# Kernel optimization log

Measured on AMD Instinct MI355X. Metric: run time of the kernel, lower is better.

Reference implementation:

```python
import jax, jax.numpy as jnp
import numpy as np


def setup_inputs() -> dict:
    key = jax.random.key(0)
    k1, k2 = jax.random.split(key)
    B, S, D, E = 4, 4096, 2048, 64
    x = jax.random.normal(k1, (B, S, D), dtype=jnp.float32)
    # nn.Linear default init ~ U(-1/sqrt(D), 1/sqrt(D)); scale down for stability
    w_gate = jax.random.normal(k2, (E, D), dtype=jnp.float32) * (1.0 / np.sqrt(D))
    expert_bias = jnp.zeros((E,), dtype=jnp.float32)
    return {"x": x, "w_gate": w_gate, "expert_bias": expert_bias}


def reference(x, w_gate, expert_bias):
    # gate_logits: [B, S, E]
    gate_logits = jnp.einsum('bsd,ed->bse', x, w_gate)
    gate_weights = jax.nn.sigmoid(gate_logits)
    biased_logits = gate_logits + expert_bias
    k = 8  # num_experts_per_tok
    _, topk_indices = jax.lax.top_k(biased_logits, k)  # [B, S, k]
    topk_weights = jnp.take_along_axis(gate_weights, topk_indices, axis=-1)
    topk_weights = topk_weights / jnp.sum(topk_weights, axis=-1, keepdims=True)
    return topk_weights, topk_indices
```

## Files before the change

kernel.cpp:

```cpp
#include <hip/hip_runtime.h>
#include <math.h>

#define DDIM 2048
#define NE 64
#define TOPK 8
#define RB 32
#define KSEG 512
#define NKT (KSEG / 32)

typedef float f32x4 __attribute__((ext_vector_type(4)));
typedef short short8 __attribute__((ext_vector_type(8)));
typedef __bf16 bf16x8 __attribute__((ext_vector_type(8)));
typedef unsigned int uint;

__device__ __forceinline__ void split3(float f, short& h, short& m, short& l) {
    uint u = __builtin_bit_cast(uint, f);
    h = (short)(u >> 16);
    float r = f - __builtin_bit_cast(float, u & 0xffff0000u);
    uint ur = __builtin_bit_cast(uint, r);
    m = (short)(ur >> 16);
    float r2 = r - __builtin_bit_cast(float, ur & 0xffff0000u);
    l = (short)(__builtin_bit_cast(uint, r2) >> 16);
}

__global__ void wsplit_kernel(const float* __restrict__ w, short* __restrict__ wh,
                              short* __restrict__ wm, short* __restrict__ wl) {
    int tid = blockIdx.x * 256 + threadIdx.x;
    size_t base = (size_t)tid * 8;
    short8 hs, ms, ls;
#pragma unroll
    for (int j = 0; j < 8; ++j) {
        short h, m, l;
        split3(w[base + j], h, m, l);
        hs[j] = h; ms[j] = m; ls[j] = l;
    }
    *(short8*)&wh[base] = hs;
    *(short8*)&wm[base] = ms;
    *(short8*)&wl[base] = ls;
}

__global__ __launch_bounds__(256, 2) void gate_kernel(
    const float* __restrict__ x,
    const float* __restrict__ bias,
    const short* __restrict__ wh,
    const short* __restrict__ wm,
    const short* __restrict__ wl,
    float* __restrict__ out_w,
    float* __restrict__ out_i)
{
    __shared__ float slab[4][RB][NE];
    __shared__ float logits[RB][NE + 1];

    const int t    = threadIdx.x;
    const int lane = t & 63;
    const int wv   = t >> 6;
    const int rl   = lane & 15;
    const int kg   = lane >> 4;
    const int row0 = blockIdx.x * RB;
    const int kbase = wv * KSEG;

    f32x4 acc[2][4];
#pragma unroll
    for (int rt = 0; rt < 2; ++rt)
#pragma unroll
        for (int et = 0; et < 4; ++et) acc[rt][et] = (f32x4){0.f, 0.f, 0.f, 0.f};

    const float* xb = x + (size_t)(row0 + rl) * DDIM + kbase + kg * 8;
    const int    wo = rl * DDIM + kbase + kg * 8;

    for (int kt = 0; kt < NKT; ++kt) {
        const int ko = kt * 32;

        bf16x8 ah[2], am[2], al[2];
#pragma unroll
        for (int rt = 0; rt < 2; ++rt) {
            const float* xp = xb + (size_t)(rt * 16) * DDIM + ko;
            f32x4 a0 = *(const f32x4*)xp;
            f32x4 a1 = *(const f32x4*)(xp + 4);
            short8 hs, ms, ls;
#pragma unroll
            for (int j = 0; j < 4; ++j) {
                short h, m, l;
                split3(a0[j], h, m, l);
                hs[j] = h; ms[j] = m; ls[j] = l;
                split3(a1[j], h, m, l);
                hs[j + 4] = h; ms[j + 4] = m; ls[j + 4] = l;
            }
            ah[rt] = __builtin_bit_cast(bf16x8, hs);
            am[rt] = __builtin_bit_cast(bf16x8, ms);
            al[rt] = __builtin_bit_cast(bf16x8, ls);
        }

#pragma unroll
        for (int et = 0; et < 4; ++et) {
            const int bofs = et * 16 * DDIM + wo + ko;
            bf16x8 bh = __builtin_bit_cast(bf16x8, *(const short8*)&wh[bofs]);
            bf16x8 bm = __builtin_bit_cast(bf16x8, *(const short8*)&wm[bofs]);
            bf16x8 bl = __builtin_bit_cast(bf16x8, *(const short8*)&wl[bofs]);
#pragma unroll
            for (int rt = 0; rt < 2; ++rt) {
                acc[rt][et] = __builtin_amdgcn_mfma_f32_16x16x32_bf16(ah[rt], bh, acc[rt][et], 0, 0, 0);
                acc[rt][et] = __builtin_amdgcn_mfma_f32_16x16x32_bf16(ah[rt], bm, acc[rt][et], 0, 0, 0);
                acc[rt][et] = __builtin_amdgcn_mfma_f32_16x16x32_bf16(am[rt], bh, acc[rt][et], 0, 0, 0);
                acc[rt][et] = __builtin_amdgcn_mfma_f32_16x16x32_bf16(am[rt], bm, acc[rt][et], 0, 0, 0);
                acc[rt][et] = __builtin_amdgcn_mfma_f32_16x16x32_bf16(ah[rt], bl, acc[rt][et], 0, 0, 0);
                acc[rt][et] = __builtin_amdgcn_mfma_f32_16x16x32_bf16(al[rt], bh, acc[rt][et], 0, 0, 0);
            }
        }
    }

#pragma unroll
    for (int rt = 0; rt < 2; ++rt)
#pragma unroll
        for (int et = 0; et < 4; ++et)
#pragma unroll
            for (int r = 0; r < 4; ++r)
                slab[wv][rt * 16 + kg * 4 + r][et * 16 + rl] = acc[rt][et][r];
    __syncthreads();

#pragma unroll
    for (int i = 0; i < 8; ++i) {
        int idx = t * 8 + i;
        int r = idx >> 6, cc = idx & 63;
        logits[r][cc] = slab[0][r][cc] + slab[1][r][cc] + slab[2][r][cc] + slab[3][r][cc];
    }
    __syncthreads();

    const float bias_l = bias[lane];
    for (int r8 = 0; r8 < 8; ++r8) {
        const int r  = wv * 8 + r8;
        const int gr = row0 + r;
        float raw = logits[r][lane];
        float sig = 1.f / (1.f + expf(-raw));
        float vv  = raw + bias_l;

        float wsum = 0.f, myw = 0.f;
        int   myidx = 0;
#pragma unroll
        for (int k = 0; k < TOPK; ++k) {
            float m = vv;
#pragma unroll
            for (int off = 32; off; off >>= 1)
                m = fmaxf(m, __shfl_xor(m, off));
            unsigned long long b = __ballot(vv == m);
            int idx = (int)__builtin_ctzll(b);
            float wk = __shfl(sig, idx);
            wsum += wk;
            if (lane == k)  { myw = wk; myidx = idx; }
            if (lane == idx) vv = -INFINITY;
        }
        if (lane < TOPK) {
            out_w[(size_t)gr * TOPK + lane] = myw / wsum;
            out_i[(size_t)gr * TOPK + lane] = (float)myidx;
        }
    }
}

extern "C" void kernel_launch(void* const* d_in, const int* in_sizes, int n_in,
                              void* d_out, int out_size, void* d_ws, size_t ws_size,
                              hipStream_t stream) {
    const float* x    = (const float*)d_in[0];
    const float* w    = (const float*)d_in[1];
    const float* bias = (const float*)d_in[2];
    const int NR = in_sizes[0] / DDIM;
    float* out   = (float*)d_out;
    float* out_w = out;
    float* out_i = out + (size_t)NR * TOPK;

    short* wh = (short*)d_ws;
    short* wm = wh + (size_t)NE * DDIM;
    short* wl = wm + (size_t)NE * DDIM;

    hipLaunchKernelGGL(wsplit_kernel, dim3(NE * DDIM / (256 * 8)), dim3(256), 0, stream,
                       w, wh, wm, wl);
    hipLaunchKernelGGL(gate_kernel, dim3(NR / RB), dim3(256), 0, stream,
                       x, bias, wh, wm, wl, out_w, out_i);
}
```

Measured before the change: 83.50 us.

## Halve row block, double-buffer loads, pad slab, interleave top-k rows

Shrinks the per-block row tile from 32 to 16, which doubles the grid so more waves are resident, and halves accumulator registers. The K loop now uses explicit double buffering: the x and split weight loads for the next step are issued before the current step's MFMAs. The slab is padded to avoid LDS bank conflicts. The top-k selection processes four rows at once so their shuffle reductions can overlap. In exchange, each weight fragment is reused across fewer rows, which doubles total weight traffic from L2, and the prefetch buffers add register pressure.

```diff
diff --git a/kernel.cpp b/kernel.cpp
--- a/kernel.cpp
+++ b/kernel.cpp
@@ -4,7 +4,7 @@
 #define DDIM 2048
 #define NE 64
 #define TOPK 8
-#define RB 32
+#define RB 16
 #define KSEG 512
 #define NKT (KSEG / 32)
 
@@ -48,7 +48,7 @@
     float* __restrict__ out_w,
     float* __restrict__ out_i)
 {
-    __shared__ float slab[4][RB][NE];
+    __shared__ float slab[4][RB][NE + 2];
     __shared__ float logits[RB][NE + 1];
 
     const int t    = threadIdx.x;
@@ -59,99 +59,115 @@
     const int row0 = blockIdx.x * RB;
     const int kbase = wv * KSEG;
 
-    f32x4 acc[2][4];
+    f32x4 acc[4];
 #pragma unroll
-    for (int rt = 0; rt < 2; ++rt)
-#pragma unroll
-        for (int et = 0; et < 4; ++et) acc[rt][et] = (f32x4){0.f, 0.f, 0.f, 0.f};
+    for (int et = 0; et < 4; ++et) acc[et] = (f32x4){0.f, 0.f, 0.f, 0.f};
 
-    const float* xb = x + (size_t)(row0 + rl) * DDIM + kbase + kg * 8;
-    const int    wo = rl * DDIM + kbase + kg * 8;
+    const float* xb  = x  + (size_t)(row0 + rl) * DDIM + kbase + kg * 8;
+    const short* whb = wh + (size_t)rl * DDIM + kbase + kg * 8;
+    const short* wmb = wm + (size_t)rl * DDIM + kbase + kg * 8;
+    const short* wlb = wl + (size_t)rl * DDIM + kbase + kg * 8;
 
-    for (int kt = 0; kt < NKT; ++kt) {
-        const int ko = kt * 32;
+    f32x4 Aa0, Aa1, Ba0, Ba1;
+    short8 Abh[4], Abm[4], Abl[4], Bbh[4], Bbm[4], Bbl[4];
 
-        bf16x8 ah[2], am[2], al[2];
-#pragma unroll
-        for (int rt = 0; rt < 2; ++rt) {
-            const float* xp = xb + (size_t)(rt * 16) * DDIM + ko;
-            f32x4 a0 = *(const f32x4*)xp;
-            f32x4 a1 = *(const f32x4*)(xp + 4);
-            short8 hs, ms, ls;
-#pragma unroll
-            for (int j = 0; j < 4; ++j) {
-                short h, m, l;
-                split3(a0[j], h, m, l);
-                hs[j] = h; ms[j] = m; ls[j] = l;
-                split3(a1[j], h, m, l);
-                hs[j + 4] = h; ms[j + 4] = m; ls[j + 4] = l;
-            }
-            ah[rt] = __builtin_bit_cast(bf16x8, hs);
-            am[rt] = __builtin_bit_cast(bf16x8, ms);
-            al[rt] = __builtin_bit_cast(bf16x8, ls);
-        }
+#define LOADT(P, ko_)                                                          \
+    {                                                                          \
+        P##a0 = *(const f32x4*)(xb + (ko_));                                   \
+        P##a1 = *(const f32x4*)(xb + (ko_) + 4);                               \
+        _Pragma("unroll")                                                      \
+        for (int et = 0; et < 4; ++et) {                                       \
+            P##bh[et] = *(const short8*)&whb[et * 16 * DDIM + (ko_)];          \
+            P##bm[et] = *(const short8*)&wmb[et * 16 * DDIM + (ko_)];          \
+            P##bl[et] = *(const short8*)&wlb[et * 16 * DDIM + (ko_)];          \
+        }                                                                      \
+    }
 
-#pragma unroll
-        for (int et = 0; et < 4; ++et) {
-            const int bofs = et * 16 * DDIM + wo + ko;
-            bf16x8 bh = __builtin_bit_cast(bf16x8, *(const short8*)&wh[bofs]);
-            bf16x8 bm = __builtin_bit_cast(bf16x8, *(const short8*)&wm[bofs]);
-            bf16x8 bl = __builtin_bit_cast(bf16x8, *(const short8*)&wl[bofs]);
-#pragma unroll
-            for (int rt = 0; rt < 2; ++rt) {
-                acc[rt][et] = __builtin_amdgcn_mfma_f32_16x16x32_bf16(ah[rt], bh, acc[rt][et], 0, 0, 0);
-                acc[rt][et] = __builtin_amdgcn_mfma_f32_16x16x32_bf16(ah[rt], bm, acc[rt][et], 0, 0, 0);
-                acc[rt][et] = __builtin_amdgcn_mfma_f32_16x16x32_bf16(am[rt], bh, acc[rt][et], 0, 0, 0);
-                acc[rt][et] = __builtin_amdgcn_mfma_f32_16x16x32_bf16(am[rt], bm, acc[rt][et], 0, 0, 0);
-                acc[rt][et] = __builtin_amdgcn_mfma_f32_16x16x32_bf16(ah[rt], bl, acc[rt][et], 0, 0, 0);
-                acc[rt][et] = __builtin_amdgcn_mfma_f32_16x16x32_bf16(al[rt], bh, acc[rt][et], 0, 0, 0);
-            }
-        }
+#define COMPUTE(P)                                                             \
+    {                                                                          \
+        short8 hs, ms, ls;                                                     \
+        _Pragma("unroll")                                                      \
+        for (int j = 0; j < 4; ++j) {                                          \
+            short h_, m_, l_;                                                  \
+            split3(P##a0[j], h_, m_, l_); hs[j] = h_; ms[j] = m_; ls[j] = l_;  \
+            split3(P##a1[j], h_, m_, l_); hs[j+4] = h_; ms[j+4] = m_; ls[j+4] = l_; \
+        }                                                                      \
+        bf16x8 ah = __builtin_bit_cast(bf16x8, hs);                            \
+        bf16x8 am = __builtin_bit_cast(bf16x8, ms);                            \
+        bf16x8 al = __builtin_bit_cast(bf16x8, ls);                            \
+        _Pragma("unroll")                                                      \
+        for (int et = 0; et < 4; ++et) {                                       \
+            bf16x8 bh = __builtin_bit_cast(bf16x8, P##bh[et]);                 \
+            bf16x8 bm = __builtin_bit_cast(bf16x8, P##bm[et]);                 \
+            bf16x8 bl = __builtin_bit_cast(bf16x8, P##bl[et]);                 \
+            acc[et] = __builtin_amdgcn_mfma_f32_16x16x32_bf16(ah, bh, acc[et], 0, 0, 0); \
+            acc[et] = __builtin_amdgcn_mfma_f32_16x16x32_bf16(ah, bm, acc[et], 0, 0, 0); \
+            acc[et] = __builtin_amdgcn_mfma_f32_16x16x32_bf16(am, bh, acc[et], 0, 0, 0); \
+            acc[et] = __builtin_amdgcn_mfma_f32_16x16x32_bf16(am, bm, acc[et], 0, 0, 0); \
+            acc[et] = __builtin_amdgcn_mfma_f32_16x16x32_bf16(ah, bl, acc[et], 0, 0, 0); \
+            acc[et] = __builtin_amdgcn_mfma_f32_16x16x32_bf16(al, bh, acc[et], 0, 0, 0); \
+        }                                                                      \
+    }
+
+    LOADT(A, 0);
+    for (int kt = 0; kt < NKT; kt += 2) {
+        LOADT(B, (kt + 1) * 32);
+        COMPUTE(A);
+        if (kt + 2 < NKT) LOADT(A, (kt + 2) * 32);
+        COMPUTE(B);
     }
 
 #pragma unroll
-    for (int rt = 0; rt < 2; ++rt)
+    for (int et = 0; et < 4; ++et)
 #pragma unroll
-        for (int et = 0; et < 4; ++et)
-#pragma unroll
-            for (int r = 0; r < 4; ++r)
-                slab[wv][rt * 16 + kg * 4 + r][et * 16 + rl] = acc[rt][et][r];
+        for (int r = 0; r < 4; ++r)
+            slab[wv][kg * 4 + r][et * 16 + rl] = acc[et][r];
     __syncthreads();
 
 #pragma unroll
-    for (int i = 0; i < 8; ++i) {
-        int idx = t * 8 + i;
+    for (int i = 0; i < 4; ++i) {
+        int idx = t * 4 + i;
         int r = idx >> 6, cc = idx & 63;
         logits[r][cc] = slab[0][r][cc] + slab[1][r][cc] + slab[2][r][cc] + slab[3][r][cc];
     }
     __syncthreads();
 
     const float bias_l = bias[lane];
-    for (int r8 = 0; r8 < 8; ++r8) {
-        const int r  = wv * 8 + r8;
-        const int gr = row0 + r;
-        float raw = logits[r][lane];
-        float sig = 1.f / (1.f + expf(-raw));
-        float vv  = raw + bias_l;
-
-        float wsum = 0.f, myw = 0.f;
-        int   myidx = 0;
+    float raw[4], sig[4], vv[4], wsum[4], myw[4];
+    int myidx[4];
 #pragma unroll
-        for (int k = 0; k < TOPK; ++k) {
-            float m = vv;
+    for (int r = 0; r < 4; ++r) {
+        raw[r] = logits[wv * 4 + r][lane];
+        sig[r] = 1.f / (1.f + expf(-raw[r]));
+        vv[r]  = raw[r] + bias_l;
+        wsum[r] = 0.f; myw[r] = 0.f; myidx[r] = 0;
+    }
 #pragma unroll
-            for (int off = 32; off; off >>= 1)
-                m = fmaxf(m, __shfl_xor(m, off));
-            unsigned long long b = __ballot(vv == m);
+    for (int k = 0; k < TOPK; ++k) {
+        float m0[4];
+#pragma unroll
+        for (int r = 0; r < 4; ++r) m0[r] = vv[r];
+#pragma unroll
+        for (int off = 32; off; off >>= 1)
+#pragma unroll
+            for (int r = 0; r < 4; ++r)
+                m0[r] = fmaxf(m0[r], __shfl_xor(m0[r], off));
+#pragma unroll
+        for (int r = 0; r < 4; ++r) {
+            unsigned long long b = __ballot(vv[r] == m0[r]);
             int idx = (int)__builtin_ctzll(b);
-            float wk = __shfl(sig, idx);
-            wsum += wk;
-            if (lane == k)  { myw = wk; myidx = idx; }
-            if (lane == idx) vv = -INFINITY;
+            float wk = __shfl(sig[r], idx);
+            wsum[r] += wk;
+            if (lane == k)   { myw[r] = wk; myidx[r] = idx; }
+            if (lane == idx) vv[r] = -INFINITY;
         }
+    }
+#pragma unroll
+    for (int r = 0; r < 4; ++r) {
         if (lane < TOPK) {
-            out_w[(size_t)gr * TOPK + lane] = myw / wsum;
-            out_i[(size_t)gr * TOPK + lane] = (float)myidx;
+            const int gr = row0 + wv * 4 + r;
+            out_w[(size_t)gr * TOPK + lane] = myw[r] / wsum[r];
+            out_i[(size_t)gr * TOPK + lane] = (float)myidx[r];
         }
     }
 }
```

Measured after the change: 115.0 us. +37.7%, slower.
